# Optimization experiments

Hardware: AMD Instinct MI355X
Metric: run time of the kernel (lower is better)

The kernel has to match this reference:

```python
import jax, jax.numpy as jnp
import numpy as np

H, D = 16, 64  # heads, head dim; E = H*D


def setup_inputs() -> dict:
    key = jax.random.key(0)
    ks = jax.random.split(key, 8)
    B, T, E = 4, 1024, 1024
    s = (2.0 / E) ** 0.5
    return {
        "x": jax.random.normal(ks[0], (B, T, E), jnp.float32),
        "wq": jax.random.normal(ks[1], (H * D, E), jnp.float32) * s,
        "wk": jax.random.normal(ks[2], (H * D, E), jnp.float32) * s,
        "wv": jax.random.normal(ks[3], (H * D, E), jnp.float32) * s,
        "wvr": jax.random.normal(ks[4], (H * D, E), jnp.float32) * s,
        "wr": jax.random.normal(ks[5], (H, E, T), jnp.float32) * s,
        "wj": jax.random.normal(ks[6], (E, E), jnp.float32) * s,
        "gate": jnp.zeros((H, 3), jnp.float32),
        "wo": jax.random.normal(ks[7], (E, H * D), jnp.float32) * s,
    }


def reference(x, wq, wk, wv, wvr, wr, wj, gate, wo):
    B, T, E = x.shape
    scale = 1.0 / D ** 0.5

    def proj(w):  # torch Linear: y = x @ w.T, then split heads -> (B,H,T,D)
        return jnp.einsum('bte,fe->btf', x, w).reshape(B, T, H, D).transpose(0, 2, 1, 3)

    mask = jnp.triu(jnp.ones((T, T), bool), 1)  # True above diagonal (masked)

    # --- branch 1: standard causal QKV attention ---
    q, k, v = proj(wq), proj(wk), proj(wv)
    s1 = jnp.einsum('bhid,bhjd->bhij', q, k) * scale
    a1 = jax.nn.softmax(jnp.where(mask, -jnp.inf, s1), axis=-1)
    out1 = jnp.einsum('bhij,bhjd->bhid', a1, v)

    # --- branch 2: RRPRAM (parameter-based per-key scores, broadcast over queries) ---
    rv = proj(wvr)
    s2 = jnp.einsum('bte,het->bht', x, wr[:, :, :T]) * scale  # score per key position
    s2 = jnp.broadcast_to(s2[:, :, None, :], (B, H, T, T))
    a2 = jax.nn.softmax(jnp.where(mask, -jnp.inf, s2), axis=-1)
    out2 = jnp.einsum('bhij,bhjd->bhid', a2, rv)

    # --- branch 3: Janus self-echo (rank-1 outer-product scores) ---
    echo = jnp.einsum('bte,fe->btf', x, wj)            # x @ wj.T
    echo_back = jnp.einsum('btf,fe->bte', echo, wj)    # echo @ wj
    sc = jnp.sum(x * echo_back, axis=-1) / (E ** 0.5)  # (B,T)
    s3 = sc[:, :, None] * sc[:, None, :]               # (B,T,T)
    a3 = jax.nn.softmax(jnp.where(mask, -jnp.inf, s3), axis=-1)
    jv = echo.reshape(B, T, H, D).transpose(0, 2, 1, 3)
    out3 = jnp.einsum('bij,bhjd->bhid', a3, jv)

    # --- gated combine (softmax over the 3 branches per head) ---
    g = jax.nn.softmax(gate, axis=-1)  # (H,3)
    out = (g[:, 0][None, :, None, None] * out1
           + g[:, 1][None, :, None, None] * out2
           + g[:, 2][None, :, None, None] * out3)
    out = out.transpose(0, 2, 1, 3).reshape(B, T, H * D)
    return jnp.einsum('btf,ef->bte', out, wo)
```

## Files before the change

### kernel.cpp

```cpp
#include <hip/hip_runtime.h>
#include <cstdint>
#include <cstddef>

typedef unsigned short u16;
typedef short bf16x8 __attribute__((ext_vector_type(8)));
typedef short bf16x4 __attribute__((ext_vector_type(4)));
typedef float f32x4 __attribute__((ext_vector_type(4)));

constexpr int B_ = 4, T_ = 1024, E_ = 1024, H_ = 16, D_ = 64;

__device__ __forceinline__ float bf2f(u16 u) {
  union { unsigned u; float f; } v; v.u = ((unsigned)u) << 16; return v.f;
}
__device__ __forceinline__ u16 f2bf(float f) {
  union { float f; unsigned u; } v; v.f = f;
  return (u16)((v.u + 0x7fffu + ((v.u >> 16) & 1u)) >> 16);
}

#define GLD_LDS16(gp, lp)                                                      \
  __builtin_amdgcn_global_load_lds(                                            \
      (const __attribute__((address_space(1))) void*)(gp),                     \
      (__attribute__((address_space(3))) void*)(lp), 16, 0, 0)

template<int WM, int WN, int MT, int NT, bool CBF16>
__global__ __launch_bounds__(WM * WN * 64) void gemm_bt(
    const u16* __restrict__ A, const u16* __restrict__ Bm,
    void* __restrict__ Cv, int N, int K,
    int lda, int ldb, int ldc,
    long batchA, long batchB, long batchC, float alpha)
{
  constexpr int TM = WM * MT * 16;
  constexpr int TN = WN * NT * 16;
  constexpr int THREADS = WM * WN * 64;
  constexpr int ASZ = TM * 32, BSZ = TN * 32;

  __shared__ u16 smem[ASZ + BSZ];
  u16* sA = smem;
  u16* sB = smem + ASZ;

  const int z = blockIdx.z;
  const u16* Ab = A + (size_t)z * batchA;
  const u16* Bb = Bm + (size_t)z * batchB;
  const int m0 = blockIdx.y * TM;
  const int n0 = blockIdx.x * TN;
  const int tid = threadIdx.x;
  const int lane = tid & 63;
  const int wave = tid >> 6;
  const int wm = wave % WM;
  const int wn = wave / WM;
  const int fr = lane & 15;
  const int fg = lane >> 4;

  f32x4 acc[MT][NT];
  const f32x4 zero = {0.f, 0.f, 0.f, 0.f};
  #pragma unroll
  for (int i = 0; i < MT; i++)
    #pragma unroll
    for (int j = 0; j < NT; j++) acc[i][j] = zero;

  for (int k0 = 0; k0 < K; k0 += 32) {
    __syncthreads();
    for (int s = tid; s < TM * 4; s += THREADS) {
      const int row = s >> 2, ch = s & 3;
      GLD_LDS16(Ab + (size_t)(m0 + row) * lda + k0 + ch * 8, &sA[s * 8]);
    }
    for (int s = tid; s < TN * 4; s += THREADS) {
      const int row = s >> 2, ch = s & 3;
      int rr = n0 + row; if (rr > N - 1) rr = N - 1;
      GLD_LDS16(Bb + (size_t)rr * ldb + k0 + ch * 8, &sB[s * 8]);
    }
    __syncthreads();

    bf16x8 av[MT], bv[NT];
    #pragma unroll
    for (int mt = 0; mt < MT; mt++)
      av[mt] = *(const bf16x8*)&sA[((wm * MT + mt) * 16 + fr) * 32 + fg * 8];
    #pragma unroll
    for (int nt = 0; nt < NT; nt++)
      bv[nt] = *(const bf16x8*)&sB[((wn * NT + nt) * 16 + fr) * 32 + fg * 8];
    #pragma unroll
    for (int mt = 0; mt < MT; mt++)
      #pragma unroll
      for (int nt = 0; nt < NT; nt++)
        acc[mt][nt] = __builtin_amdgcn_mfma_f32_16x16x32_bf16(av[mt], bv[nt], acc[mt][nt], 0, 0, 0);
  }

  const int er = (lane >> 4) * 4;
  const int ec = lane & 15;
  #pragma unroll
  for (int mt = 0; mt < MT; mt++) {
    #pragma unroll
    for (int nt = 0; nt < NT; nt++) {
      const int row = m0 + (wm * MT + mt) * 16 + er;
      const int col = n0 + (wn * NT + nt) * 16 + ec;
      if (col < N) {
        #pragma unroll
        for (int r2 = 0; r2 < 4; r2++) {
          const float vv = acc[mt][nt][r2] * alpha;
          const size_t ci = (size_t)z * batchC + (size_t)(row + r2) * ldc + col;
          if constexpr (CBF16) ((u16*)Cv)[ci] = f2bf(vv);
          else                 ((float*)Cv)[ci] = vv;
        }
      }
    }
  }
}

__global__ __launch_bounds__(256) void gemm_echo(
    const u16* __restrict__ A, const u16* __restrict__ Alo,
    const u16* __restrict__ Bm, const u16* __restrict__ Blo,
    u16* __restrict__ echoT, float* __restrict__ sc)
{
  constexpr int TM = 128, TN = 64;
  constexpr int ASZ = TM * 32, BSZ = TN * 32;
  __shared__ u16 smem[2 * (ASZ + BSZ)];
  u16* sA  = smem;
  u16* sB  = smem + ASZ;
  u16* sAl = smem + ASZ + BSZ;
  u16* sBl = smem + 2 * ASZ + BSZ;

  const int m0 = blockIdx.y * TM;
  const int n0 = blockIdx.x * TN;
  const int tid = threadIdx.x;
  const int lane = tid & 63;
  const int wave = tid >> 6;
  const int wm = wave % 2;
  const int wn = wave / 2;
  const int fr = lane & 15, fg = lane >> 4;

  f32x4 acc[4][2];
  #pragma unroll
  for (int i = 0; i < 4; i++)
    #pragma unroll
    for (int j = 0; j < 2; j++) acc[i][j] = f32x4{0.f, 0.f, 0.f, 0.f};

  for (int k0 = 0; k0 < E_; k0 += 32) {
    __syncthreads();
    for (int s = tid; s < TM * 4; s += 256) {
      const int row = s >> 2, ch = s & 3;
      const size_t go = (size_t)(m0 + row) * E_ + k0 + ch * 8;
      GLD_LDS16(A + go, &sA[s * 8]);
      GLD_LDS16(Alo + go, &sAl[s * 8]);
    }
    for (int s = tid; s < TN * 4; s += 256) {
      const int row = s >> 2, ch = s & 3;
      const size_t go = (size_t)(n0 + row) * E_ + k0 + ch * 8;
      GLD_LDS16(Bm + go, &sB[s * 8]);
      GLD_LDS16(Blo + go, &sBl[s * 8]);
    }
    __syncthreads();

    bf16x8 av[4], bv[2], al[4], bl[2];
    #pragma unroll
    for (int mt = 0; mt < 4; mt++) {
      av[mt] = *(const bf16x8*)&sA[((wm * 4 + mt) * 16 + fr) * 32 + fg * 8];
      al[mt] = *(const bf16x8*)&sAl[((wm * 4 + mt) * 16 + fr) * 32 + fg * 8];
    }
    #pragma unroll
    for (int nt = 0; nt < 2; nt++) {
      bv[nt] = *(const bf16x8*)&sB[((wn * 2 + nt) * 16 + fr) * 32 + fg * 8];
      bl[nt] = *(const bf16x8*)&sBl[((wn * 2 + nt) * 16 + fr) * 32 + fg * 8];
    }
    #pragma unroll
    for (int mt = 0; mt < 4; mt++)
      #pragma unroll
      for (int nt = 0; nt < 2; nt++) {
        acc[mt][nt] = __builtin_amdgcn_mfma_f32_16x16x32_bf16(av[mt], bv[nt], acc[mt][nt], 0, 0, 0);
        acc[mt][nt] = __builtin_amdgcn_mfma_f32_16x16x32_bf16(al[mt], bv[nt], acc[mt][nt], 0, 0, 0);
        acc[mt][nt] = __builtin_amdgcn_mfma_f32_16x16x32_bf16(av[mt], bl[nt], acc[mt][nt], 0, 0, 0);
      }
  }

  __syncthreads();
  const int b   = m0 >> 10;
  const int t0l = m0 & 1023;
  const int ec  = lane & 15;
  u16* lt = smem;

  #pragma unroll
  for (int mt = 0; mt < 4; mt++) {
    float sq[4] = {0.f, 0.f, 0.f, 0.f};
    #pragma unroll
    for (int nt = 0; nt < 2; nt++) {
      const int cl = (wn * 2 + nt) * 16 + ec;
      #pragma unroll
      for (int r2 = 0; r2 < 4; r2++) {
        const float vv = acc[mt][nt][r2];
        sq[r2] += vv * vv;
        lt[cl * 132 + (wm * 4 + mt) * 16 + fg * 4 + r2] = f2bf(vv);
      }
    }
    #pragma unroll
    for (int m2 = 1; m2 < 16; m2 <<= 1) {
      sq[0] += __shfl_xor(sq[0], m2, 64);
      sq[1] += __shfl_xor(sq[1], m2, 64);
      sq[2] += __shfl_xor(sq[2], m2, 64);
      sq[3] += __shfl_xor(sq[3], m2, 64);
    }
    if (ec == 0) {
      #pragma unroll
      for (int r2 = 0; r2 < 4; r2++)
        atomicAdd(&sc[(size_t)b * T_ + t0l + (wm * 4 + mt) * 16 + fg * 4 + r2], sq[r2]);
    }
  }
  __syncthreads();
  for (int s = tid; s < 64 * 128; s += 256) {
    const int f = s >> 7, t = s & 127;
    echoT[((size_t)b * E_ + n0 + f) * T_ + t0l + t] = lt[f * 132 + t];
  }
}

__global__ __launch_bounds__(256, 2) void flash1(
    const u16* __restrict__ qkvr, const u16* __restrict__ vTb, u16* __restrict__ out1) {
  const int it = blockIdx.x, h = blockIdx.y, b = blockIdx.z;
  const int tid = threadIdx.x, lane = tid & 63, w = tid >> 6;
  const int fr = lane & 15, fg = lane >> 4;

  __shared__ u16 sQ[8192];
  __shared__ u16 sK[8192];
  __shared__ u16 sV[8192];

  const u16* Qb = qkvr + ((size_t)(b * T_) + it * 128) * 4096 + h * 64;
  const u16* Kb = qkvr + (size_t)(b * T_) * 4096 + 1024 + h * 64;
  const u16* Vb = vTb + (size_t)(b * H_ + h) * (D_ * T_);

  for (int s = tid; s < 1024; s += 256) {
    const int l = s & 63, g = s >> 6;
    const int row = (g >> 1) * 16 + (l & 15);
    const int c8  = (g & 1) * 4 + (l >> 4);
    GLD_LDS16(Qb + (size_t)row * 4096 + c8 * 8, &sQ[s * 8]);
  }
  __syncthreads();

  bf16x8 bQ[2][2];
  #pragma unroll
  for (int mf = 0; mf < 2; mf++)
    #pragma unroll
    for (int kk = 0; kk < 2; kk++)
      bQ[mf][kk] = *(const bf16x8*)&sQ[((((w * 2 + mf) * 2 + kk) << 6) | lane) * 8];

  f32x4 accO[2][4];
  float mrow[2], lrow[2];
  #pragma unroll
  for (int mf = 0; mf < 2; mf++) {
    mrow[mf] = -3.0e38f; lrow[mf] = 0.f;
    #pragma unroll
    for (int nd = 0; nd < 4; nd++) accO[mf][nd] = f32x4{0.f, 0.f, 0.f, 0.f};
  }

  for (int jt = 0; jt <= it; jt++) {
    __syncthreads();
    for (int s = tid; s < 1024; s += 256) {
      const int l = s & 63, g = s >> 6;
      const int row = (g >> 1) * 16 + (l & 15);
      const int c8  = (g & 1) * 4 + (l >> 4);
      GLD_LDS16(Kb + (size_t)(jt * 128 + row) * 4096 + c8 * 8, &sK[s * 8]);
    }
    for (int s = tid; s < 1024; s += 256) {
      const int jc = s >> 6, d = s & 63;
      GLD_LDS16(Vb + ((size_t)(jt * 16 + jc)) * 512 + d * 8, &sV[s * 8]);
    }
    __syncthreads();

    f32x4 accST[2][8];
    #pragma unroll
    for (int mf = 0; mf < 2; mf++)
      #pragma unroll
      for (int nf = 0; nf < 8; nf++) accST[mf][nf] = f32x4{0.f, 0.f, 0.f, 0.f};
    #pragma unroll
    for (int kk = 0; kk < 2; kk++) {
      #pragma unroll
      for (int nf = 0; nf < 8; nf++) {
        const bf16x8 aK = *(const bf16x8*)&sK[((((nf << 1) | kk) << 6) | lane) * 8];
        accST[0][nf] = __builtin_amdgcn_mfma_f32_16x16x32_bf16(aK, bQ[0][kk], accST[0][nf], 0, 0, 0);
        accST[1][nf] = __builtin_amdgcn_mfma_f32_16x16x32_bf16(aK, bQ[1][kk], accST[1][nf], 0, 0, 0);
      }
    }

    const bool diag = (jt == it);
    bf16x4 pf[2][8];
    #pragma unroll
    for (int mf = 0; mf < 2; mf++) {
      const int iloc = w * 32 + mf * 16 + fr;
      float sv[8][4];
      float rmax = -3.0e38f;
      #pragma unroll
      for (int nf = 0; nf < 8; nf++)
        #pragma unroll
        for (int r = 0; r < 4; r++) {
          float s = accST[mf][nf][r] * 0.125f;
          if (diag && (nf * 16 + fg * 4 + r) > iloc) s = -3.0e38f;
          sv[nf][r] = s;
          rmax = fmaxf(rmax, s);
        }
      rmax = fmaxf(rmax, __shfl_xor(rmax, 16, 64));
      rmax = fmaxf(rmax, __shfl_xor(rmax, 32, 64));
      const float mn = fmaxf(mrow[mf], rmax);
      const float al = __expf(mrow[mf] - mn);
      mrow[mf] = mn;
      float ps = 0.f;
      #pragma unroll
      for (int nf = 0; nf < 8; nf++)
        #pragma unroll
        for (int r = 0; r < 4; r++) {
          const float pv = __expf(sv[nf][r] - mn);
          ps += pv;
          pf[mf][nf][r] = (short)f2bf(pv);
        }
      ps += __shfl_xor(ps, 16, 64);
      ps += __shfl_xor(ps, 32, 64);
      lrow[mf] = lrow[mf] * al + ps;
      #pragma unroll
      for (int r = 0; r < 4; r++) {
        const float alr = __shfl(al, fg * 4 + r, 64);
        #pragma unroll
        for (int nd = 0; nd < 4; nd++) accO[mf][nd][r] *= alr;
      }
    }

    #pragma unroll
    for (int kc = 0; kc < 8; kc++) {
      bf16x8 bV[4];
      #pragma unroll
      for (int nd = 0; nd < 4; nd++) {
        const bf16x4 vv = *(const bf16x4*)&sV[
            (((kc * 2 + (fg >> 1)) * 64 + nd * 16 + fr) * 8) + (fg & 1) * 4];
        bV[nd] = bf16x8{vv[0], vv[1], vv[2], vv[3], 0, 0, 0, 0};
      }
      #pragma unroll
      for (int mf = 0; mf < 2; mf++) {
        const bf16x4 pp = pf[mf][kc];
        const bf16x8 pA = bf16x8{pp[0], pp[1], pp[2], pp[3], 0, 0, 0, 0};
        #pragma unroll
        for (int nd = 0; nd < 4; nd++)
          accO[mf][nd] = __builtin_amdgcn_mfma_f32_16x16x32_bf16(pA, bV[nd], accO[mf][nd], 0, 0, 0);
      }
    }
  }

  u16* op = out1 + ((size_t)(b * T_) + it * 128) * E_ + h * 64;
  #pragma unroll
  for (int mf = 0; mf < 2; mf++) {
    const float li = 1.0f / lrow[mf];
    #pragma unroll
    for (int r = 0; r < 4; r++) {
      const float linv = __shfl(li, fg * 4 + r, 64);
      const int row = w * 32 + mf * 16 + fg * 4 + r;
      #pragma unroll
      for (int nd = 0; nd < 4; nd++)
        op[(size_t)row * E_ + nd * 16 + fr] = f2bf(accO[mf][nd][r] * linv);
    }
  }
}

__device__ __forceinline__ float block_max256(float v, float* red) {
  #pragma unroll
  for (int m = 32; m > 0; m >>= 1) v = fmaxf(v, __shfl_xor(v, m, 64));
  if ((threadIdx.x & 63) == 0) red[threadIdx.x >> 6] = v;
  __syncthreads();
  const float r = fmaxf(fmaxf(red[0], red[1]), fmaxf(red[2], red[3]));
  __syncthreads();
  return r;
}
__device__ __forceinline__ float block_sum256(float v, float* red) {
  #pragma unroll
  for (int m = 32; m > 0; m >>= 1) v += __shfl_xor(v, m, 64);
  if ((threadIdx.x & 63) == 0) red[threadIdx.x >> 6] = v;
  __syncthreads();
  const float r = (red[0] + red[1]) + (red[2] + red[3]);
  __syncthreads();
  return r;
}

__global__ __launch_bounds__(256) void cast_all(
    const float* __restrict__ x, const float* __restrict__ wq,
    const float* __restrict__ wk, const float* __restrict__ wv,
    const float* __restrict__ wvr, const float* __restrict__ wo,
    const float* __restrict__ wj,
    u16* __restrict__ xb, u16* __restrict__ xlo, u16* __restrict__ wcat,
    u16* __restrict__ wob, u16* __restrict__ wjb, u16* __restrict__ wjlo) {
  const int bid = blockIdx.x;
  if (bid < 4096) {
    const size_t i = ((size_t)bid * 256 + threadIdx.x) * 4;
    const float4 v = *(const float4*)(x + i);
    ushort4 oh, ol;
    oh.x = f2bf(v.x); ol.x = f2bf(v.x - bf2f(oh.x));
    oh.y = f2bf(v.y); ol.y = f2bf(v.y - bf2f(oh.y));
    oh.z = f2bf(v.z); ol.z = f2bf(v.z - bf2f(oh.z));
    oh.w = f2bf(v.w); ol.w = f2bf(v.w - bf2f(oh.w));
    *(ushort4*)(xb + i) = oh;
    *(ushort4*)(xlo + i) = ol;
  } else if (bid < 8192) {
    const int r = (bid - 4096) >> 10;
    const float* src = (r == 0) ? wq : (r == 1) ? wk : (r == 2) ? wv : wvr;
    const size_t i = ((size_t)((bid - 4096) & 1023) * 256 + threadIdx.x) * 4;
    const float4 v = *(const float4*)(src + i);
    ushort4 o;
    o.x = f2bf(v.x); o.y = f2bf(v.y); o.z = f2bf(v.z); o.w = f2bf(v.w);
    *(ushort4*)(wcat + (size_t)r * (1 << 20) + i) = o;
  } else if (bid < 9216) {
    const size_t i = ((size_t)(bid - 8192) * 256 + threadIdx.x) * 4;
    const float4 v = *(const float4*)(wo + i);
    ushort4 o;
    o.x = f2bf(v.x); o.y = f2bf(v.y); o.z = f2bf(v.z); o.w = f2bf(v.w);
    *(ushort4*)(wob + i) = o;
  } else {
    const size_t i = ((size_t)(bid - 9216) * 256 + threadIdx.x) * 4;
    const float4 v = *(const float4*)(wj + i);
    ushort4 oh, ol;
    oh.x = f2bf(v.x); ol.x = f2bf(v.x - bf2f(oh.x));
    oh.y = f2bf(v.y); ol.y = f2bf(v.y - bf2f(oh.y));
    oh.z = f2bf(v.z); ol.z = f2bf(v.z - bf2f(oh.z));
    oh.w = f2bf(v.w); ol.w = f2bf(v.w - bf2f(oh.w));
    *(ushort4*)(wjb + i) = oh;
    *(ushort4*)(wjlo + i) = ol;
  }
}

__global__ __launch_bounds__(256) void s2_direct(
    const u16* __restrict__ xb, const float* __restrict__ wr, float* __restrict__ s2) {
  const int t0 = blockIdx.x * 32, h = blockIdx.y;
  const int tt = threadIdx.x & 31, eg = threadIdx.x >> 5;
  float acc[4] = {0.f, 0.f, 0.f, 0.f};
  const float* wp = wr + (size_t)h * E_ * T_ + t0 + tt;
  for (int ec = 0; ec < 8; ec++) {
    const int e0 = ec * 128 + eg * 16;
    bf16x8 xv[4][2];
    #pragma unroll
    for (int b = 0; b < 4; b++) {
      const u16* xp = xb + ((size_t)(b * T_) + t0 + tt) * E_ + e0;
      xv[b][0] = *(const bf16x8*)xp;
      xv[b][1] = *(const bf16x8*)(xp + 8);
    }
    #pragma unroll
    for (int e2 = 0; e2 < 16; e2++) {
      const float w = wp[(size_t)(e0 + e2) * T_];
      #pragma unroll
      for (int b = 0; b < 4; b++)
        acc[b] += bf2f((u16)xv[b][e2 >> 3][e2 & 7]) * w;
    }
  }
  __shared__ float red[8][4][33];
  #pragma unroll
  for (int b = 0; b < 4; b++) red[eg][b][tt] = acc[b];
  __syncthreads();
  if (threadIdx.x < 128) {
    const int b = threadIdx.x >> 5, t = threadIdx.x & 31;
    float s = 0.f;
    #pragma unroll
    for (int g = 0; g < 8; g++) s += red[g][b][t];
    s2[((size_t)b * H_ + h) * T_ + t0 + t] = s * 0.125f;
  }
}

__global__ __launch_bounds__(256) void a3_softmax(const float* __restrict__ sc, u16* __restrict__ a3) {
  const int i = blockIdx.x;
  const int b = blockIdx.y;
  const float* sr = sc + (size_t)b * T_;
  const float sci = sr[i] * 0.03125f;
  u16* row = a3 + ((size_t)b * T_ + i) * T_;
  __shared__ float red[4];
  float v[4];
  float m = -3.0e38f;
  #pragma unroll
  for (int k = 0; k < 4; k++) {
    const int j = threadIdx.x + k * 256;
    const float xv = (j <= i) ? sci * (sr[j] * 0.03125f) : -3.0e38f;
    v[k] = xv;
    m = fmaxf(m, xv);
  }
  m = block_max256(m, red);
  float s = 0.f;
  #pragma unroll
  for (int k = 0; k < 4; k++) {
    const int j = threadIdx.x + k * 256;
    const float p = (j <= i) ? __expf(v[k] - m) : 0.f;
    v[k] = p;
    s += p;
  }
  s = block_sum256(s, red);
  const float inv = 1.0f / s;
  #pragma unroll
  for (int k = 0; k < 4; k++) {
    const int j = threadIdx.x + k * 256;
    row[j] = f2bf(v[k] * inv);
  }
}

__global__ __launch_bounds__(1024) void branch2_scan(
    const float* __restrict__ s2, const u16* __restrict__ rv, int ldrv,
    u16* __restrict__ out2) {
  const int h = blockIdx.x, b = blockIdx.y;
  const int tid = threadIdx.x;
  const int lane = tid & 63;
  const int wv = tid >> 6;

  const float* srow = s2 + ((size_t)b * H_ + h) * T_;

  __shared__ float wbuf[T_];
  __shared__ float numtot[16][64];
  __shared__ float dentot[16];
  __shared__ float redm[16];

  float m = srow[tid];
  #pragma unroll
  for (int mk = 32; mk > 0; mk >>= 1) m = fmaxf(m, __shfl_xor(m, mk, 64));
  if (lane == 0) redm[wv] = m;
  __syncthreads();
  m = redm[0];
  #pragma unroll
  for (int i2 = 1; i2 < 16; i2++) m = fmaxf(m, redm[i2]);

  wbuf[tid] = __expf(srow[tid] - m);
  __syncthreads();

  const u16* rvp = rv + (size_t)(b * T_) * ldrv + h * D_ + lane;
  const int j0 = wv * 64;
  float num = 0.f, den = 0.f;
  #pragma unroll 8
  for (int j2 = 0; j2 < 64; j2++) {
    const float w = wbuf[j0 + j2];
    den += w;
    num += w * bf2f(rvp[(size_t)(j0 + j2) * ldrv]);
  }
  numtot[wv][lane] = num;
  if (lane == 0) dentot[wv] = den;
  __syncthreads();

  float num_off = 0.f, den_off = 0.f;
  for (int w2 = 0; w2 < wv; w2++) {
    num_off += numtot[w2][lane];
    den_off += dentot[w2];
  }

  u16* op = out2 + (size_t)b * T_ * E_ + h * D_ + lane;
  num = num_off; den = den_off;
  #pragma unroll 8
  for (int j2 = 0; j2 < 64; j2++) {
    const float w = wbuf[j0 + j2];
    num += w * bf2f(rvp[(size_t)(j0 + j2) * ldrv]);
    den += w;
    op[(size_t)(j0 + j2) * E_] = f2bf(num / den);
  }
}

__global__ __launch_bounds__(256) void transpose_v(const u16* __restrict__ v, u16* __restrict__ vTb,
                                                   int ldv) {
  const int bh = blockIdx.x;
  const int b = bh >> 4, h = bh & 15;
  const int d0 = blockIdx.y * 32, t0 = blockIdx.z * 32;
  __shared__ u16 tile[32][33];
  const int c = threadIdx.x & 31, r0 = threadIdx.x >> 5;
  #pragma unroll
  for (int rr = 0; rr < 32; rr += 8) {
    const int t = t0 + rr + r0;
    tile[rr + r0][c] = v[((size_t)b * T_ + t) * ldv + h * 64 + d0 + c];
  }
  __syncthreads();
  #pragma unroll
  for (int rr = 0; rr < 32; rr += 8) {
    const int d = d0 + rr + r0;
    const int t = t0 + c;
    vTb[((size_t)(bh * 128 + (t >> 3)) * 64 + d) * 8 + (t & 7)] = tile[c][rr + r0];
  }
}

__global__ __launch_bounds__(256) void combine_gate(
    const u16* __restrict__ o1, const u16* __restrict__ o2, const u16* __restrict__ o3,
    const float* __restrict__ gate, u16* __restrict__ comb) {
  const size_t idx = (size_t)blockIdx.x * 256 + threadIdx.x;
  const int f = (int)(idx & (E_ - 1));
  const int h = f >> 6;
  const float g0 = gate[h * 3 + 0], g1 = gate[h * 3 + 1], g2 = gate[h * 3 + 2];
  const float mx = fmaxf(g0, fmaxf(g1, g2));
  const float e0 = __expf(g0 - mx), e1 = __expf(g1 - mx), e2 = __expf(g2 - mx);
  const float inv = 1.0f / (e0 + e1 + e2);
  const float o = (e0 * bf2f(o1[idx]) + e1 * bf2f(o2[idx]) + e2 * bf2f(o3[idx])) * inv;
  comb[idx] = f2bf(o);
}

extern "C" void kernel_launch(void* const* d_in, const int* in_sizes, int n_in,
                              void* d_out, int out_size, void* d_ws, size_t ws_size,
                              hipStream_t stream) {
  (void)in_sizes; (void)n_in; (void)out_size; (void)ws_size;
  const float* x    = (const float*)d_in[0];
  const float* wq   = (const float*)d_in[1];
  const float* wk   = (const float*)d_in[2];
  const float* wv   = (const float*)d_in[3];
  const float* wvr  = (const float*)d_in[4];
  const float* wr   = (const float*)d_in[5];
  const float* wj   = (const float*)d_in[6];
  const float* gate = (const float*)d_in[7];
  const float* wo   = (const float*)d_in[8];
  float* out = (float*)d_out;

  char* p = (char*)d_ws;
  auto alloc = [&](size_t bytes) -> char* {
    char* r = p; p += (bytes + 255) & ~(size_t)255; return r;
  };
  const size_t NTE = (size_t)B_ * T_ * E_;
  const size_t NW  = (size_t)E_ * E_;

  u16* xb    = (u16*)alloc(NTE * 2);
  u16* xlo   = (u16*)alloc(NTE * 2);
  u16* wcat  = (u16*)alloc(4 * NW * 2);
  u16* wjb   = (u16*)alloc(NW * 2);
  u16* wjlo  = (u16*)alloc(NW * 2);
  u16* wob   = (u16*)alloc(NW * 2);
  u16* qkvr  = (u16*)alloc(NTE * 4 * 2);
  u16* vT    = (u16*)alloc(NTE * 2);
  u16* echoT = (u16*)alloc(NTE * 2);
  u16* a3p   = (u16*)alloc(NTE * 2);
  float* sc  = (float*)alloc((size_t)B_ * T_ * 4);
  float* s2  = (float*)alloc((size_t)B_ * H_ * T_ * 4);
  u16* out1b = (u16*)alloc(NTE * 2);
  u16* out2b = (u16*)alloc(NTE * 2);
  u16* out3b = (u16*)alloc(NTE * 2);
  u16* comb  = (u16*)alloc(NTE * 2);

  cast_all<<<dim3(10240), 256, 0, stream>>>(x, wq, wk, wv, wvr, wo, wj,
                                            xb, xlo, wcat, wob, wjb, wjlo);
  hipMemsetAsync(sc, 0, (size_t)B_ * T_ * 4, stream);

  gemm_bt<2,2,4,4,true><<<dim3(32, 32, 1), 256, 0, stream>>>(
      xb, wcat, qkvr, 4096, E_, E_, E_, 4096, 0L, 0L, 0L, 1.f);

  gemm_echo<<<dim3(16, 32, 1), 256, 0, stream>>>(xb, xlo, wjb, wjlo, echoT, sc);

  transpose_v<<<dim3(B_ * H_, D_ / 32, T_ / 32), 256, 0, stream>>>(qkvr + 2048, vT, 4096);
  s2_direct<<<dim3(T_ / 32, H_), 256, 0, stream>>>(xb, wr, s2);

  branch2_scan<<<dim3(H_, B_), 1024, 0, stream>>>(s2, qkvr + 3072, 4096, out2b);

  a3_softmax<<<dim3(T_, B_), 256, 0, stream>>>(sc, a3p);
  gemm_bt<2,2,4,2,true><<<dim3(E_ / 64, T_ / 128, B_), 256, 0, stream>>>(
      a3p, echoT, out3b, E_, T_, T_, T_, E_,
      (long)T_ * T_, (long)E_ * T_, (long)T_ * E_, 1.f);

  flash1<<<dim3(T_ / 128, H_, B_), 256, 0, stream>>>(qkvr, vT, out1b);

  combine_gate<<<dim3((unsigned)(NTE / 256)), 256, 0, stream>>>(out1b, out2b, out3b, gate, comb);
  gemm_bt<2,2,4,2,false><<<dim3(E_ / 64, (B_ * T_) / 128, 1), 256, 0, stream>>>(
      comb, wob, out, E_, E_, E_, E_, E_, 0L, 0L, 0L, 1.f);
}
```

Baseline: 394.2 us.

## Replace QKV projection GEMM with 256x256-tile 8-wave pipelined MFMA kernel

Adds a dedicated QKV projection GEMM that uses 256x256 output tiles with 8 waves and a double-buffered 128KB LDS. It streams K slices in quarter-stages via global_load_lds with an XOR swizzle, and interleaves those stage loads with MFMA phases using explicit barriers, waitcnt and setprio. The aim is higher data reuse and overlap of global loads with compute compared with the generic 128x128 gemm_bt. In exchange, the large LDS footprint limits occupancy to one block per CU and the grid shrinks to 256 blocks, which may underfill the GPU.

```diff
diff --git a/kernel.cpp b/kernel.cpp
--- a/kernel.cpp
+++ b/kernel.cpp
@@ -21,6 +21,161 @@
   __builtin_amdgcn_global_load_lds(                                            \
       (const __attribute__((address_space(1))) void*)(gp),                     \
       (__attribute__((address_space(3))) void*)(lp), 16, 0, 0)
+
+#define SBAR()                                                                 \
+  do {                                                                         \
+    __builtin_amdgcn_sched_barrier(0);                                         \
+    __builtin_amdgcn_s_barrier();                                              \
+    __builtin_amdgcn_sched_barrier(0);                                         \
+  } while (0)
+#define WAIT_LGKM0()                                                           \
+  do {                                                                         \
+    asm volatile("s_waitcnt lgkmcnt(0)" ::: "memory");                         \
+    __builtin_amdgcn_sched_barrier(0);                                         \
+  } while (0)
+#define WAIT_VM6()                                                             \
+  do {                                                                         \
+    asm volatile("s_waitcnt vmcnt(6)" ::: "memory");                           \
+    __builtin_amdgcn_sched_barrier(0);                                         \
+  } while (0)
+
+__global__ __launch_bounds__(512) void gemm_qkv8(
+    const u16* __restrict__ A, const u16* __restrict__ Bm, u16* __restrict__ C)
+{
+  __shared__ u16 smem[65536];
+
+  const int tid  = threadIdx.x;
+  const int lane = tid & 63;
+  const int wave = tid >> 6;
+  const int wm = wave >> 2;
+  const int wn = wave & 3;
+  const int fr = lane & 15;
+  const int fg = lane >> 4;
+  const int fx = fr & 7;
+  const int m0 = blockIdx.y * 256;
+  const int n0 = blockIdx.x * 256;
+
+  auto stage = [&](int g) {
+    const int half = g & 3;
+    const int buf  = (g >> 2) & 1;
+    int kt = g >> 2; if (kt > 15) kt = 15;
+    const int k0 = kt << 6;
+    const u16* src = (half < 2)
+        ? (A  + (size_t)(m0 + (half & 1) * 128) * 1024)
+        : (Bm + (size_t)(n0 + (half & 1) * 128) * 1024);
+    u16* dst = smem + (buf << 15) + (half << 13);
+    #pragma unroll
+    for (int l = 0; l < 2; l++) {
+      const int s = (l << 9) | tid;
+      const int r = s >> 3, ch = s & 7;
+      GLD_LDS16(src + (size_t)r * 1024 + k0 + ((ch ^ (r & 7)) << 3), dst + s * 8);
+    }
+  };
+
+  f32x4 acc[8][4];
+  #pragma unroll
+  for (int i = 0; i < 8; i++)
+    #pragma unroll
+    for (int j = 0; j < 4; j++) acc[i][j] = f32x4{0.f, 0.f, 0.f, 0.f};
+
+  #pragma unroll
+  for (int g = 0; g < 7; g++) stage(g);
+  WAIT_VM6();
+  __builtin_amdgcn_s_barrier();
+  __builtin_amdgcn_sched_barrier(0);
+
+  const int ko0 = (fg ^ fx) << 3;
+  const int ko1 = ((4 | fg) ^ fx) << 3;
+
+  bf16x8 aF[8][2], bF[4][2];
+
+  #pragma unroll 2
+  for (int t = 0; t < 16; t++) {
+    const int buf = t & 1;
+    const int ab = (buf << 15) + (wm << 13) + fr * 64;
+    const int bb = (buf << 15) + 16384 + ((wn >> 1) << 13) + ((wn & 1) << 12) + fr * 64;
+
+    #pragma unroll
+    for (int mt = 0; mt < 8; mt++) {
+      aF[mt][0] = *(const bf16x8*)(smem + ab + mt * 1024 + ko0);
+      aF[mt][1] = *(const bf16x8*)(smem + ab + mt * 1024 + ko1);
+    }
+    #pragma unroll
+    for (int nt = 0; nt < 2; nt++) {
+      bF[nt][0] = *(const bf16x8*)(smem + bb + nt * 1024 + ko0);
+      bF[nt][1] = *(const bf16x8*)(smem + bb + nt * 1024 + ko1);
+    }
+    stage(4 * t + 7);
+    SBAR();
+    WAIT_LGKM0();
+    __builtin_amdgcn_s_setprio(1);
+    #pragma unroll
+    for (int mt = 0; mt < 4; mt++)
+      #pragma unroll
+      for (int nt = 0; nt < 2; nt++) {
+        acc[mt][nt] = __builtin_amdgcn_mfma_f32_16x16x32_bf16(aF[mt][0], bF[nt][0], acc[mt][nt], 0, 0, 0);
+        acc[mt][nt] = __builtin_amdgcn_mfma_f32_16x16x32_bf16(aF[mt][1], bF[nt][1], acc[mt][nt], 0, 0, 0);
+      }
+    __builtin_amdgcn_s_setprio(0);
+    SBAR();
+
+    #pragma unroll
+    for (int nt = 2; nt < 4; nt++) {
+      bF[nt][0] = *(const bf16x8*)(smem + bb + nt * 1024 + ko0);
+      bF[nt][1] = *(const bf16x8*)(smem + bb + nt * 1024 + ko1);
+    }
+    stage(4 * t + 8);
+    SBAR();
+    WAIT_LGKM0();
+    __builtin_amdgcn_s_setprio(1);
+    #pragma unroll
+    for (int mt = 0; mt < 4; mt++)
+      #pragma unroll
+      for (int nt = 2; nt < 4; nt++) {
+        acc[mt][nt] = __builtin_amdgcn_mfma_f32_16x16x32_bf16(aF[mt][0], bF[nt][0], acc[mt][nt], 0, 0, 0);
+        acc[mt][nt] = __builtin_amdgcn_mfma_f32_16x16x32_bf16(aF[mt][1], bF[nt][1], acc[mt][nt], 0, 0, 0);
+      }
+    __builtin_amdgcn_s_setprio(0);
+    SBAR();
+
+    stage(4 * t + 9);
+    SBAR();
+    __builtin_amdgcn_s_setprio(1);
+    #pragma unroll
+    for (int mt = 4; mt < 8; mt++)
+      #pragma unroll
+      for (int nt = 0; nt < 2; nt++) {
+        acc[mt][nt] = __builtin_amdgcn_mfma_f32_16x16x32_bf16(aF[mt][0], bF[nt][0], acc[mt][nt], 0, 0, 0);
+        acc[mt][nt] = __builtin_amdgcn_mfma_f32_16x16x32_bf16(aF[mt][1], bF[nt][1], acc[mt][nt], 0, 0, 0);
+      }
+    __builtin_amdgcn_s_setprio(0);
+    SBAR();
+
+    stage(4 * t + 10);
+    SBAR();
+    __builtin_amdgcn_s_setprio(1);
+    #pragma unroll
+    for (int mt = 4; mt < 8; mt++)
+      #pragma unroll
+      for (int nt = 2; nt < 4; nt++) {
+        acc[mt][nt] = __builtin_amdgcn_mfma_f32_16x16x32_bf16(aF[mt][0], bF[nt][0], acc[mt][nt], 0, 0, 0);
+        acc[mt][nt] = __builtin_amdgcn_mfma_f32_16x16x32_bf16(aF[mt][1], bF[nt][1], acc[mt][nt], 0, 0, 0);
+      }
+    __builtin_amdgcn_s_setprio(0);
+    WAIT_VM6();
+    __builtin_amdgcn_s_barrier();
+    __builtin_amdgcn_sched_barrier(0);
+  }
+
+  u16* Cp = C + (size_t)(m0 + wm * 128) * 4096 + n0 + wn * 64;
+  #pragma unroll
+  for (int mt = 0; mt < 8; mt++)
+    #pragma unroll
+    for (int nt = 0; nt < 4; nt++)
+      #pragma unroll
+      for (int r2 = 0; r2 < 4; r2++)
+        Cp[(size_t)(mt * 16 + fg * 4 + r2) * 4096 + nt * 16 + fr] = f2bf(acc[mt][nt][r2]);
+}
 
 template<int WM, int WN, int MT, int NT, bool CBF16>
 __global__ __launch_bounds__(WM * WN * 64) void gemm_bt(
@@ -622,8 +777,7 @@
                                             xb, xlo, wcat, wob, wjb, wjlo);
   hipMemsetAsync(sc, 0, (size_t)B_ * T_ * 4, stream);
 
-  gemm_bt<2,2,4,4,true><<<dim3(32, 32, 1), 256, 0, stream>>>(
-      xb, wcat, qkvr, 4096, E_, E_, E_, 4096, 0L, 0L, 0L, 1.f);
+  gemm_qkv8<<<dim3(16, 16), 512, 0, stream>>>(xb, wcat, qkvr);
 
   gemm_echo<<<dim3(16, 32, 1), 256, 0, stream>>>(xb, xlo, wjb, wjlo, echoT, sc);
 
```

New measurement: 388.7 us. About the same (-1.4%).
